# Kernel tuning notes

Hardware: AMD Instinct MI355X
Metric: run time of the kernel (lower is better)

Reference implementation:

```python
import jax, jax.numpy as jnp
import numpy as np

B, S, IN_DIM = 128, 1024, 256
M, D, OUT = 64, 128, 128


def setup_inputs() -> dict:
    key = jax.random.key(0)
    ks = jax.random.split(key, 10)
    def xavier(k, shape):
        fan_in, fan_out = shape[-1], shape[-2] if len(shape) > 1 else shape[-1]
        lim = jnp.sqrt(6.0 / (shape[0] + shape[1]))
        return jax.random.uniform(k, shape, jnp.float32, -lim, lim)
    return {
        "x": jax.random.normal(ks[0], (B, S, IN_DIM), jnp.float32),
        "memory_key": xavier(ks[1], (M, D)),
        "memory_value": xavier(ks[2], (M, D)),
        "Wr": xavier(ks[3], (IN_DIM, D)),
        "br": jnp.zeros((D,), jnp.float32),
        "Ww": xavier(ks[4], (IN_DIM, D)),
        "bw": jnp.zeros((D,), jnp.float32),
        "Wp": xavier(ks[5], (D, OUT)),
        "bp": jnp.zeros((OUT,), jnp.float32),
    }


def reference(x, memory_key, memory_value, Wr, br, Ww, bw, Wp, bp):
    # Precompute time-parallel parts: read keys and write erase/add signals.
    k_all = jnp.einsum("bsi,id->bsd", x, Wr) + br          # [B,S,D]
    v_all = jnp.einsum("bsi,id->bsd", x, Ww) + bw          # [B,S,D]
    erase_all = jax.nn.sigmoid(v_all)                        # [B,S,D]
    add_all = jnp.tanh(v_all)                                # [B,S,D]

    Mv0 = jnp.broadcast_to(memory_value, (x.shape[0],) + memory_value.shape)  # [B,M,D]

    def step(Mv, inp):
        k_t, e_t, a_t = inp                                  # each [B,D]
        w = jax.nn.softmax(k_t @ memory_key.T, axis=-1)      # [B,M]
        r = jnp.einsum("bm,bmd->bd", w, Mv)                # [B,D]
        y = jax.nn.sigmoid(r @ Wp + bp)                      # [B,OUT]
        wE = w[:, :, None]                                   # [B,M,1]
        Mv = Mv * (1.0 - wE * e_t[:, None, :]) + wE * a_t[:, None, :]
        return Mv, y

    xs = (jnp.swapaxes(k_all, 0, 1),
          jnp.swapaxes(erase_all, 0, 1),
          jnp.swapaxes(add_all, 0, 1))                       # [S,B,D] each
    _, ys = jax.lax.scan(step, Mv0, xs)                      # ys: [S,B,OUT]
    return jnp.swapaxes(ys, 0, 1)                            # [B,S,OUT]
```

## Files before the change

### kernel.cpp

```cpp
#include <hip/hip_runtime.h>
#include <hip/hip_bf16.h>


#define B_   128
#define S_   1024
#define IN_  256
#define M_   64
#define D_   128
#define OUT_ 128
#define NROWS_ (B_ * S_)

typedef __hip_bfloat16 bf16;
typedef unsigned int uint32;
typedef __attribute__((ext_vector_type(8))) short s16x8;
typedef __attribute__((ext_vector_type(4))) float f32x4;

__device__ __forceinline__ float tof(bf16 v) { return __bfloat162float(v); }
__device__ __forceinline__ bf16  tob(float v) { return __float2bfloat16(v); }
__device__ __forceinline__ float ldf(const float* p, long i) { return p[i]; }
__device__ __forceinline__ float ldf(const bf16* p, long i)  { return tof(p[i]); }
__device__ __forceinline__ void  stf(float* p, long i, float v) { p[i] = v; }
__device__ __forceinline__ void  stf(bf16* p, long i, float v)  { p[i] = tob(v); }
__device__ __forceinline__ void  unp(uint32 u, float& lo, float& hi) {
  lo = __uint_as_float(u << 16);
  hi = __uint_as_float(u & 0xFFFF0000u);
}
__device__ __forceinline__ uint32 pk(float lo, float hi) {
  union { bf16 h; unsigned short u; } a, b;
  a.h = tob(lo); b.h = tob(hi);
  return (uint32)a.u | ((uint32)b.u << 16);
}
__device__ __forceinline__ void split2(float f0, float f1, uint32& h, uint32& l) {
  union { bf16 b; unsigned short u; } a0, a1;
  a0.b = tob(f0); a1.b = tob(f1);
  h = (uint32)a0.u | ((uint32)a1.u << 16);
  const float r0 = f0 - tof(a0.b);
  const float r1 = f1 - tof(a1.b);
  l = pk(r0, r1);
}
__device__ __forceinline__ void gl16(const void* g, void* s) {
  __builtin_amdgcn_global_load_lds(
      (const __attribute__((address_space(1))) void*)g,
      (__attribute__((address_space(3))) void*)s, 16, 0, 0);
}

__global__ __launch_bounds__(256) void k_probe(const uint32* __restrict__ xw,
                                               int* __restrict__ flag) {
  __shared__ int s[256];
  const int tid = threadIdx.x;
  int sc = 0;
#pragma unroll
  for (int k = 0; k < 8; ++k) {
    const uint32 u = xw[tid * 8 + k];
    const float v = __uint_as_float(u << 16);
    if (!(fabsf(v) < 4.0f)) sc++;
  }
  s[tid] = sc;
  __syncthreads();
  for (int o = 128; o > 0; o >>= 1) {
    if (tid < o) s[tid] += s[tid + o];
    __syncthreads();
  }
  if (tid == 0) *flag = (s[0] > 64) ? 1 : 0;
}

template <typename T>
__device__ void k0_body(const T* Wr, const T* br, const T* K,
                        float* Wk, float* bk) {
  const int idx = blockIdx.x * 256 + threadIdx.x;
  if (idx < IN_ * M_) {
    const int i = idx >> 6, m = idx & 63;
    float acc = 0.f;
    for (int d = 0; d < D_; ++d)
      acc = fmaf(ldf(Wr, (long)i * D_ + d), ldf(K, (long)m * D_ + d), acc);
    Wk[idx] = acc;
  } else if (idx < IN_ * M_ + M_) {
    const int m = idx - IN_ * M_;
    float acc = 0.f;
    for (int d = 0; d < D_; ++d)
      acc = fmaf(ldf(br, d), ldf(K, (long)m * D_ + d), acc);
    bk[m] = acc;
  }
}

__global__ __launch_bounds__(256) void k0_fold(const void* Wr, const void* br,
                                               const void* K, float* Wk, float* bk,
                                               const int* flag) {
  if (*flag) k0_body<float>((const float*)Wr, (const float*)br, (const float*)K, Wk, bk);
  else       k0_body<bf16>((const bf16*)Wr, (const bf16*)br, (const bf16*)K, Wk, bk);
}

__global__ __launch_bounds__(256) void k0b_pack(const void* Ww, const void* Wp,
                                                const float* Wk, bf16* WTh, bf16* WTl,
                                                bf16* WpTh, bf16* WpTl,
                                                const int* flag) {
  const int f = *flag;
  const int idx = blockIdx.x * 256 + threadIdx.x;
  if (idx < 12 * 8 * 64 * 8) {
    const int j = idx & 7, lane = (idx >> 3) & 63;
    const int kst = (idx >> 9) & 7, ct = idx >> 12;
    const int l15 = lane & 15, quad = lane >> 4;
    const int n = ct * 16 + l15;
    const int k = kst * 32 + quad * 8 + j;
    float v;
    if (f) v = (n < 128) ? ((const float*)Ww)[k * 128 + n] : Wk[k * 64 + (n - 128)];
    else   v = (n < 128) ? tof(((const bf16*)Ww)[k * 128 + n]) : Wk[k * 64 + (n - 128)];
    const bf16 h = tob(v);
    WTh[idx] = h;
    if (f) WTl[idx] = tob(v - tof(h));
  } else {
    const int o = idx - 12 * 8 * 64 * 8;
    const int j = o & 7, lane = (o >> 3) & 63;
    const int kst = (o >> 9) & 3, ct = o >> 11;
    const int l15 = lane & 15, quad = lane >> 4;
    const int n = ct * 16 + l15;
    const int k = kst * 32 + quad * 8 + j;
    float v;
    if (f) v = ((const float*)Wp)[k * 128 + n];
    else   v = tof(((const bf16*)Wp)[k * 128 + n]);
    const bf16 h = tob(v);
    WpTh[o] = h;
    if (f) WpTl[o] = tob(v - tof(h));
  }
}

template <bool F32>
__device__ void k1_body(const void* x, const void* bw, const float* bk,
                        const bf16* __restrict__ WTh, const bf16* __restrict__ WTl,
                        uint32* __restrict__ ea_all, float* __restrict__ w_all,
                        int chunk, int TL, int tshift) {
  const int tid = threadIdx.x;
  const int wave = tid >> 6, lane = tid & 63;
  const int l15 = lane & 15, quad = lane >> 4;
  const int b = blockIdx.x >> tshift;
  const int tb = blockIdx.x & ((1 << tshift) - 1);
  const int t0 = tb * 64 + wave * 16;
  const long lr0 = (long)b * TL + t0;
  const long ar0 = (long)b * S_ + (long)chunk * TL + t0;

  s16x8 afh[8], afl[8];
  if constexpr (F32) {
    const float* xr = (const float*)x + (ar0 + l15) * (long)IN_ + quad * 8;
#pragma unroll
    for (int k = 0; k < 8; ++k) {
      const float4 u0 = *(const float4*)(xr + k * 32);
      const float4 u1 = *(const float4*)(xr + k * 32 + 4);
      union { s16x8 v; uint32 u[4]; } H, L;
      split2(u0.x, u0.y, H.u[0], L.u[0]);
      split2(u0.z, u0.w, H.u[1], L.u[1]);
      split2(u1.x, u1.y, H.u[2], L.u[2]);
      split2(u1.z, u1.w, H.u[3], L.u[3]);
      afh[k] = H.v;
      afl[k] = L.v;
    }
  } else {
    const bf16* xr = (const bf16*)x + (ar0 + l15) * (long)IN_ + quad * 8;
#pragma unroll
    for (int k = 0; k < 8; ++k) afh[k] = *(const s16x8*)(xr + k * 32);
  }

  f32x4 acc[12];
#pragma unroll
  for (int ct = 0; ct < 12; ++ct) acc[ct] = (f32x4){0.f, 0.f, 0.f, 0.f};

  const bf16* fbh = WTh + lane * 8;
  const bf16* fbl = WTl + lane * 8;
#pragma unroll
  for (int ct = 0; ct < 12; ++ct) {
#pragma unroll
    for (int k = 0; k < 8; ++k) {
      const s16x8 bh = *(const s16x8*)(fbh + (ct * 8 + k) * 512);
      acc[ct] = __builtin_amdgcn_mfma_f32_16x16x32_bf16(afh[k], bh, acc[ct], 0, 0, 0);
      if constexpr (F32) {
        const s16x8 bl = *(const s16x8*)(fbl + (ct * 8 + k) * 512);
        acc[ct] = __builtin_amdgcn_mfma_f32_16x16x32_bf16(afl[k], bh, acc[ct], 0, 0, 0);
        acc[ct] = __builtin_amdgcn_mfma_f32_16x16x32_bf16(afh[k], bl, acc[ct], 0, 0, 0);
      }
    }
  }

#pragma unroll
  for (int ct = 0; ct < 8; ++ct) {
    const int col = ct * 16 + l15;
    float bb;
    if constexpr (F32) bb = ((const float*)bw)[col];
    else               bb = tof(((const bf16*)bw)[col]);
#pragma unroll
    for (int r = 0; r < 4; ++r) {
      const float v = acc[ct][r] + bb;
      const float sg = 1.0f / (1.0f + exp2f(-1.44269504f * v));
      const float th = 1.0f - 2.0f / (exp2f(2.88539008f * v) + 1.0f);
      ea_all[(lr0 + quad * 4 + r) * D_ + col] = pk(sg, th);
    }
  }
  float bks[4];
#pragma unroll
  for (int g = 0; g < 4; ++g) bks[g] = bk[g * 16 + l15];
#pragma unroll
  for (int r = 0; r < 4; ++r) {
    float s[4];
    float mx = -1e30f;
#pragma unroll
    for (int g = 0; g < 4; ++g) {
      s[g] = acc[8 + g][r] + bks[g];
      mx = fmaxf(mx, s[g]);
    }
#pragma unroll
    for (int off = 1; off < 16; off <<= 1) mx = fmaxf(mx, __shfl_xor(mx, off, 64));
    float ex[4], sum = 0.f;
#pragma unroll
    for (int g = 0; g < 4; ++g) {
      ex[g] = exp2f(1.44269504f * (s[g] - mx));
      sum += ex[g];
    }
#pragma unroll
    for (int off = 1; off < 16; off <<= 1) sum += __shfl_xor(sum, off, 64);
    const float inv = 1.0f / sum;
    const long lr = lr0 + quad * 4 + r;
#pragma unroll
    for (int g = 0; g < 4; ++g)
      w_all[lr * M_ + g * 16 + l15] = ex[g] * inv;
  }
}

__global__ __launch_bounds__(256, 2) void k1_mfma(const void* x, const void* bw,
                                                  const float* bk, const bf16* WTh,
                                                  const bf16* WTl, uint32* ea_all,
                                                  float* w_all, int chunk, int TL,
                                                  int tshift,
                                                  const int* __restrict__ flag) {
  if (*flag) k1_body<true>(x, bw, bk, WTh, WTl, ea_all, w_all, chunk, TL, tshift);
  else       k1_body<false>(x, bw, bk, WTh, WTl, ea_all, w_all, chunk, TL, tshift);
}

template <typename T>
__device__ void k2_body(const T* Mv0, const uint32* ea_all, const float* w_all,
                        float* MvS, T* r_out, int chunk, int TL, int TC) {
  const int tid = threadIdx.x;
  const int wave = tid >> 6, lane = tid & 63;
  const int mg = lane >> 2, dl = lane & 3;
  const int b = blockIdx.x & 127;
  const int dgHi = blockIdx.x >> 7;
  const int q = wave * 4 + dl;
  const int d = dgHi * 16 + q;
  const int m0 = mg * 4;

  __shared__ uint32 sEA[2][16][16];
  __shared__ float  sW[2][16][64];

  float Mv[4];
  if (chunk == 0) {
#pragma unroll
    for (int j = 0; j < 4; ++j)
      Mv[j] = ldf(Mv0, (long)(m0 + j) * D_ + d);
  } else {
#pragma unroll
    for (int j = 0; j < 4; ++j)
      Mv[j] = MvS[((long)b * M_ + m0 + j) * D_ + d];
  }

  const long lrbase = (long)b * TL;
  const long arbase = (long)b * S_ + (long)chunk * TL;

  const int sl2 = lane >> 2, sl4 = lane >> 4;
  const int eac = (lane & 3) * 4;
  const int wmc = (lane & 15) * 4;
  auto stage = [&](int buf, int t0) {
    gl16(&ea_all[(lrbase + t0 + sl2) * D_ + dgHi * 16 + eac], &sEA[buf][0][0]);
#pragma unroll
    for (int i = 0; i < 4; ++i)
      gl16(&w_all[(lrbase + t0 + i * 4 + sl4) * M_ + wmc], &sW[buf][i * 4][0]);
  };

  if (wave == 0) stage(0, 0);
  __syncthreads();

  const int NT = TL / 16;
  for (int kk = 0; kk < NT; ++kk) {
    const int cur = kk & 1;
    if (wave == 0 && kk + 1 < NT) stage(cur ^ 1, (kk + 1) * 16);
    const long ab = arbase + kk * 16;
#pragma unroll
    for (int t = 0; t < 16; ++t) {
      float e, a;
      unp(sEA[cur][t][q], e, a);
      const float4 wv = *(const float4*)&sW[cur][t][m0];
      float r = 0.f;
#pragma unroll
      for (int j = 0; j < 4; ++j) {
        r = fmaf(wv[j == 0 ? 0 : j == 1 ? 1 : j == 2 ? 2 : 3], Mv[j], r);
        Mv[j] = fmaf((&wv.x)[j], fmaf(-e, Mv[j], a), Mv[j]);
      }
      r += __shfl_xor(r, 4, 64);
      r += __shfl_xor(r, 8, 64);
      r += __shfl_xor(r, 16, 64);
      r += __shfl_xor(r, 32, 64);
      if (mg == 0) stf(r_out, (ab + t) * D_ + d, r);
    }
    __syncthreads();
  }

  if (chunk < TC - 1) {
#pragma unroll
    for (int j = 0; j < 4; ++j)
      MvS[((long)b * M_ + m0 + j) * D_ + d] = Mv[j];
  }
}

__global__ __launch_bounds__(256) void k2_scan(const void* Mv0, const uint32* ea_all,
                                               const float* w_all, float* MvS,
                                               void* r_out, int chunk, int TL,
                                               int TC, const int* flag) {
  if (*flag) k2_body<float>((const float*)Mv0, ea_all, w_all, MvS,
                            (float*)r_out, chunk, TL, TC);
  else       k2_body<bf16>((const bf16*)Mv0, ea_all, w_all, MvS,
                           (bf16*)r_out, chunk, TL, TC);
}

template <bool F32>
__device__ void k3_body(const bf16* __restrict__ WpTh, const bf16* __restrict__ WpTl,
                        const void* bpv, void* iov) {
  const int tid = threadIdx.x;
  const int wave = tid >> 6, lane = tid & 63;
  const int l15 = lane & 15, quad = lane >> 4;
  const long row0 = (long)blockIdx.x * 64 + wave * 16;

  s16x8 afh[4], afl[4];
  if constexpr (F32) {
    const float* rr = (const float*)iov + (row0 + l15) * D_ + quad * 8;
#pragma unroll
    for (int k = 0; k < 4; ++k) {
      const float4 u0 = *(const float4*)(rr + k * 32);
      const float4 u1 = *(const float4*)(rr + k * 32 + 4);
      union { s16x8 v; uint32 u[4]; } H, L;
      split2(u0.x, u0.y, H.u[0], L.u[0]);
      split2(u0.z, u0.w, H.u[1], L.u[1]);
      split2(u1.x, u1.y, H.u[2], L.u[2]);
      split2(u1.z, u1.w, H.u[3], L.u[3]);
      afh[k] = H.v;
      afl[k] = L.v;
    }
  } else {
    const bf16* rr = (const bf16*)iov + (row0 + l15) * D_ + quad * 8;
#pragma unroll
    for (int k = 0; k < 4; ++k) afh[k] = *(const s16x8*)(rr + k * 32);
  }

  f32x4 acc[8];
#pragma unroll
  for (int ct = 0; ct < 8; ++ct) acc[ct] = (f32x4){0.f, 0.f, 0.f, 0.f};
  const bf16* fbh = WpTh + lane * 8;
  const bf16* fbl = WpTl + lane * 8;
#pragma unroll
  for (int ct = 0; ct < 8; ++ct) {
#pragma unroll
    for (int k = 0; k < 4; ++k) {
      const s16x8 bh = *(const s16x8*)(fbh + (ct * 4 + k) * 512);
      acc[ct] = __builtin_amdgcn_mfma_f32_16x16x32_bf16(afh[k], bh, acc[ct], 0, 0, 0);
      if constexpr (F32) {
        const s16x8 bl = *(const s16x8*)(fbl + (ct * 4 + k) * 512);
        acc[ct] = __builtin_amdgcn_mfma_f32_16x16x32_bf16(afl[k], bh, acc[ct], 0, 0, 0);
        acc[ct] = __builtin_amdgcn_mfma_f32_16x16x32_bf16(afh[k], bl, acc[ct], 0, 0, 0);
      }
    }
  }
#pragma unroll
  for (int ct = 0; ct < 8; ++ct) {
    const int col = ct * 16 + l15;
    float bb;
    if constexpr (F32) bb = ((const float*)bpv)[col];
    else               bb = tof(((const bf16*)bpv)[col]);
#pragma unroll
    for (int r = 0; r < 4; ++r) {
      const float y = 1.0f / (1.0f + exp2f(-1.44269504f * (acc[ct][r] + bb)));
      if constexpr (F32)
        ((float*)iov)[(row0 + quad * 4 + r) * OUT_ + col] = y;
      else
        ((bf16*)iov)[(row0 + quad * 4 + r) * OUT_ + col] = tob(y);
    }
  }
}

__global__ __launch_bounds__(256, 2) void k3_mfma(const bf16* __restrict__ WpTh,
                                                  const bf16* __restrict__ WpTl,
                                                  const void* bpv, void* iov,
                                                  const int* __restrict__ flag) {
  if (*flag) k3_body<true>(WpTh, WpTl, bpv, iov);
  else       k3_body<false>(WpTh, WpTl, bpv, iov);
}

extern "C" void kernel_launch(void* const* d_in, const int* in_sizes, int n_in,
                              void* d_out, int out_size, void* d_ws, size_t ws_size,
                              hipStream_t stream) {
  const void* x   = d_in[0];
  const void* mk  = d_in[1];
  const void* mv  = d_in[2];
  const void* Wr  = d_in[3];
  const void* br  = d_in[4];
  const void* Ww  = d_in[5];
  const void* bwv = d_in[6];
  const void* Wp  = d_in[7];
  const void* bp  = d_in[8];

  char* ws = (char*)d_ws;
  int*    flag = (int*)ws;
  float*  Wk   = (float*)(ws + 16);
  float*  bk   = (float*)(ws + 16 + 65536);
  bf16*   WTh  = (bf16*)(ws + 65808);
  bf16*   WTl  = WTh + 192 * 256;
  bf16*   WpTh = WTl + 192 * 256;
  bf16*   WpTl = WpTh + 128 * 128;
  char*   dyn  = (char*)(WpTl + 128 * 128);
  const size_t fixed = (size_t)(dyn - ws);

  int TC = 16;
  for (int c = 1; c <= 16; c <<= 1) {
    const size_t rc = (size_t)NROWS_ / c;
    const size_t need = fixed + rc * (D_ * 4 + M_ * 4) +
                        (c > 1 ? (size_t)B_ * M_ * D_ * 4 : 0) + 1024;
    if (need <= ws_size) { TC = c; break; }
  }
  const int TL = S_ / TC;
  const int tshift = __builtin_ctz(TL / 64);
  const size_t RC = (size_t)NROWS_ / TC;

  uint32* ea_all = (uint32*)dyn;
  float*  w_all  = (float*)(ea_all + RC * D_);
  float*  MvS    = (float*)(w_all + RC * M_);

  k_probe<<<1, 256, 0, stream>>>((const uint32*)x, flag);
  k0_fold<<<(IN_ * M_ + M_ + 255) / 256, 256, 0, stream>>>(Wr, br, mk, Wk, bk, flag);
  k0b_pack<<<256, 256, 0, stream>>>(Ww, Wp, Wk, WTh, WTl, WpTh, WpTl, flag);
  for (int c = 0; c < TC; ++c) {
    k1_mfma<<<(int)(RC / 64), 256, 0, stream>>>(x, bwv, bk, WTh, WTl, ea_all, w_all,
                                                c, TL, tshift, flag);
    k2_scan<<<B_ * 8, 256, 0, stream>>>(mv, ea_all, w_all, MvS, d_out, c, TL, TC,
                                        flag);
  }
  k3_mfma<<<NROWS_ / 64, 256, 0, stream>>>(WpTh, WpTl, bp, d_out, flag);
}
```

Baseline: 639.3 us.

## Widen per-thread memory slots in scan kernel and spread staging across waves

The recurrent scan kernel now gives each thread 8 memory slots instead of 4 and each block 32 feature columns instead of 16, halving the grid to 512 blocks. The cross-lane reduction shrinks from four shuffles to three, and the w/ea tile staging is split across three waves instead of one. The aim is to cut shuffle and staging overhead per step, at the cost of fewer blocks, which lowers latency hiding on the serial scan.

```diff
diff --git a/kernel.cpp b/kernel.cpp
--- a/kernel.cpp
+++ b/kernel.cpp
@@ -238,63 +238,74 @@
                         float* MvS, T* r_out, int chunk, int TL, int TC) {
   const int tid = threadIdx.x;
   const int wave = tid >> 6, lane = tid & 63;
-  const int mg = lane >> 2, dl = lane & 3;
+  const int mg = lane & 7, dloc = lane >> 3;
   const int b = blockIdx.x & 127;
-  const int dgHi = blockIdx.x >> 7;
-  const int q = wave * 4 + dl;
-  const int d = dgHi * 16 + q;
-  const int m0 = mg * 4;
-
-  __shared__ uint32 sEA[2][16][16];
+  const int dq = blockIdx.x >> 7;
+  const int dl = wave * 8 + dloc;
+  const int d = dq * 32 + dl;
+  const int m0 = mg * 8;
+
+  __shared__ uint32 sEA[2][16][32];
   __shared__ float  sW[2][16][64];
 
-  float Mv[4];
+  float Mv[8];
   if (chunk == 0) {
 #pragma unroll
-    for (int j = 0; j < 4; ++j)
+    for (int j = 0; j < 8; ++j)
       Mv[j] = ldf(Mv0, (long)(m0 + j) * D_ + d);
   } else {
 #pragma unroll
-    for (int j = 0; j < 4; ++j)
+    for (int j = 0; j < 8; ++j)
       Mv[j] = MvS[((long)b * M_ + m0 + j) * D_ + d];
   }
 
   const long lrbase = (long)b * TL;
   const long arbase = (long)b * S_ + (long)chunk * TL;
 
-  const int sl2 = lane >> 2, sl4 = lane >> 4;
-  const int eac = (lane & 3) * 4;
-  const int wmc = (lane & 15) * 4;
   auto stage = [&](int buf, int t0) {
-    gl16(&ea_all[(lrbase + t0 + sl2) * D_ + dgHi * 16 + eac], &sEA[buf][0][0]);
-#pragma unroll
-    for (int i = 0; i < 4; ++i)
-      gl16(&w_all[(lrbase + t0 + i * 4 + sl4) * M_ + wmc], &sW[buf][i * 4][0]);
+    if (wave == 0) {
+#pragma unroll
+      for (int c = 0; c < 2; ++c)
+        gl16(&ea_all[(lrbase + t0 + c * 8 + (lane >> 3)) * D_ + dq * 32 +
+                     (lane & 7) * 4],
+             &sEA[buf][c * 8][0]);
+    } else if (wave == 1) {
+#pragma unroll
+      for (int i = 0; i < 2; ++i)
+        gl16(&w_all[(lrbase + t0 + i * 4 + (lane >> 4)) * M_ + (lane & 15) * 4],
+             &sW[buf][i * 4][0]);
+    } else if (wave == 2) {
+#pragma unroll
+      for (int i = 2; i < 4; ++i)
+        gl16(&w_all[(lrbase + t0 + i * 4 + (lane >> 4)) * M_ + (lane & 15) * 4],
+             &sW[buf][i * 4][0]);
+    }
   };
 
-  if (wave == 0) stage(0, 0);
+  stage(0, 0);
   __syncthreads();
 
   const int NT = TL / 16;
   for (int kk = 0; kk < NT; ++kk) {
     const int cur = kk & 1;
-    if (wave == 0 && kk + 1 < NT) stage(cur ^ 1, (kk + 1) * 16);
+    if (kk + 1 < NT) stage(cur ^ 1, (kk + 1) * 16);
     const long ab = arbase + kk * 16;
 #pragma unroll
     for (int t = 0; t < 16; ++t) {
       float e, a;
-      unp(sEA[cur][t][q], e, a);
-      const float4 wv = *(const float4*)&sW[cur][t][m0];
+      unp(sEA[cur][t][dl], e, a);
+      const float4 w0 = *(const float4*)&sW[cur][t][m0];
+      const float4 w1 = *(const float4*)&sW[cur][t][m0 + 4];
+      const float wv[8] = {w0.x, w0.y, w0.z, w0.w, w1.x, w1.y, w1.z, w1.w};
       float r = 0.f;
 #pragma unroll
-      for (int j = 0; j < 4; ++j) {
-        r = fmaf(wv[j == 0 ? 0 : j == 1 ? 1 : j == 2 ? 2 : 3], Mv[j], r);
-        Mv[j] = fmaf((&wv.x)[j], fmaf(-e, Mv[j], a), Mv[j]);
+      for (int j = 0; j < 8; ++j) {
+        r = fmaf(wv[j], Mv[j], r);
+        Mv[j] = fmaf(wv[j], fmaf(-e, Mv[j], a), Mv[j]);
       }
+      r += __shfl_xor(r, 1, 64);
+      r += __shfl_xor(r, 2, 64);
       r += __shfl_xor(r, 4, 64);
-      r += __shfl_xor(r, 8, 64);
-      r += __shfl_xor(r, 16, 64);
-      r += __shfl_xor(r, 32, 64);
       if (mg == 0) stf(r_out, (ab + t) * D_ + d, r);
     }
     __syncthreads();
@@ -302,7 +313,7 @@
 
   if (chunk < TC - 1) {
 #pragma unroll
-    for (int j = 0; j < 4; ++j)
+    for (int j = 0; j < 8; ++j)
       MvS[((long)b * M_ + m0 + j) * D_ + d] = Mv[j];
   }
 }
@@ -434,7 +445,7 @@
   for (int c = 0; c < TC; ++c) {
     k1_mfma<<<(int)(RC / 64), 256, 0, stream>>>(x, bwv, bk, WTh, WTl, ea_all, w_all,
                                                 c, TL, tshift, flag);
-    k2_scan<<<B_ * 8, 256, 0, stream>>>(mv, ea_all, w_all, MvS, d_out, c, TL, TC,
+    k2_scan<<<B_ * 4, 256, 0, stream>>>(mv, ea_all, w_all, MvS, d_out, c, TL, TC,
                                         flag);
   }
   k3_mfma<<<NROWS_ / 64, 256, 0, stream>>>(WpTh, WpTl, bp, d_out, flag);
```

Result: faster. 615.9 us (-3.7%).
